# Optimization experiments

Measured on AMD Instinct MI355X. Metric: run time of the kernel, lower is better.

The kernel has to match this reference:

```python
import jax, jax.numpy as jnp
import numpy as np

N_EMBD = 2048
N_HEAD = 16
N_KV_HEAD = 4
HEAD_DIM = 128
KV_REPEATS = N_HEAD // N_KV_HEAD
ROPE_THETA = 10000.0


def rotate_half(x):
    # interleaved pair rotation: (x0,x1,x2,x3,...) -> (-x1,x0,-x3,x2,...)
    x_even = x[..., 0::2]
    x_odd = x[..., 1::2]
    return jnp.stack((-x_odd, x_even), axis=-1).reshape(x.shape)


def apply_rope(q, k, position_ids):
    inv_freq = 1.0 / (ROPE_THETA ** (jnp.arange(0, HEAD_DIM, 2, dtype=jnp.float32) / HEAD_DIM))
    freqs = position_ids.astype(jnp.float32)[:, None] * inv_freq[None, :]  # [S, D/2]
    emb = jnp.repeat(freqs, 2, axis=-1)  # [S, D] interleaved
    cos = jnp.cos(emb)[None, None, :, :]
    sin = jnp.sin(emb)[None, None, :, :]
    return q * cos + rotate_half(q) * sin, k * cos + rotate_half(k) * sin


def setup_inputs() -> dict:
    key = jax.random.key(0)
    ks = jax.random.split(key, 5)
    B, S = 2, 2048
    x = jax.random.normal(ks[0], (B, S, N_EMBD), dtype=jnp.float32)
    position_ids = jnp.arange(S, dtype=jnp.int32)
    scale = 0.02
    Wq = jax.random.normal(ks[1], (N_HEAD * HEAD_DIM, N_EMBD), dtype=jnp.float32) * scale
    Wk = jax.random.normal(ks[2], (N_KV_HEAD * HEAD_DIM, N_EMBD), dtype=jnp.float32) * scale
    Wv = jax.random.normal(ks[3], (N_KV_HEAD * HEAD_DIM, N_EMBD), dtype=jnp.float32) * scale
    Wo = jax.random.normal(ks[4], (N_EMBD, N_EMBD), dtype=jnp.float32) * scale
    return {"x": x, "Wq": Wq, "Wk": Wk, "Wv": Wv, "Wo": Wo, "position_ids": position_ids}


def reference(x, Wq, Wk, Wv, Wo, position_ids):
    B, S, _ = x.shape
    q = (x @ Wq.T).reshape(B, S, N_HEAD, HEAD_DIM).transpose(0, 2, 1, 3)      # [B,H,S,D]
    k = (x @ Wk.T).reshape(B, S, N_KV_HEAD, HEAD_DIM).transpose(0, 2, 1, 3)  # [B,Hkv,S,D]
    v = (x @ Wv.T).reshape(B, S, N_KV_HEAD, HEAD_DIM).transpose(0, 2, 1, 3)
    q, k = apply_rope(q, k, position_ids)
    # GQA: repeat kv heads consecutively
    k = jnp.repeat(k, KV_REPEATS, axis=1)  # [B,H,S,D]
    v = jnp.repeat(v, KV_REPEATS, axis=1)
    scores = jnp.einsum('bhqd,bhkd->bhqk', q, k) / jnp.sqrt(jnp.asarray(HEAD_DIM, q.dtype))
    key_positions = jnp.arange(S)
    mask = key_positions[None, :] > position_ids[:, None]  # [S, S]
    scores = jnp.where(mask[None, None, :, :], jnp.finfo(scores.dtype).min, scores)
    weights = jax.nn.softmax(scores.astype(jnp.float32), axis=-1).astype(q.dtype)
    y = jnp.einsum('bhqk,bhkd->bhqd', weights, v)
    y = y.transpose(0, 2, 1, 3).reshape(B, S, N_EMBD)
    return y @ Wo.T
```

## Files before the change

### kernel.cpp

```cpp
#include <hip/hip_runtime.h>
#include <stdint.h>

typedef unsigned short u16;
typedef unsigned int   u32;
typedef __attribute__((ext_vector_type(8))) short short8;
typedef __attribute__((ext_vector_type(4))) float f32x4;

#define S_LEN 2048
#define NEMB  2048
#define NH    16
#define NKV   4
#define HD    128
#define BATCH 2
#define MROWS (BATCH*S_LEN)

#define SCALE_Q 0.12751744f

__device__ __forceinline__ u16 f2bf(float f){
  u32 u = __float_as_uint(f);
  u += 0x7fffu + ((u>>16)&1u);
  return (u16)(u>>16);
}
__device__ __forceinline__ u16 f2bf_t(float f){
  return (u16)(__float_as_uint(f)>>16);
}
__device__ __forceinline__ float bf2f(u16 h){
  return __uint_as_float(((u32)h)<<16);
}
__device__ __forceinline__ float exp2_fast(float x){
  float r;
  asm("v_exp_f32 %0, %1" : "=v"(r) : "v"(x));
  return r;
}

typedef __attribute__((address_space(1))) const void gc_void;
typedef __attribute__((address_space(3))) void lds_void;
__device__ __forceinline__ void load_lds16(const void* g, void* l){
  __builtin_amdgcn_global_load_lds((gc_void*)(uintptr_t)g,
      (lds_void*)(u32)(uintptr_t)l, 16, 0, 0);
}

__global__ __launch_bounds__(256) void convert_kernel(
    const float* __restrict__ x, const float* __restrict__ wq,
    const float* __restrict__ wk, const float* __restrict__ wv,
    const float* __restrict__ wo,
    u16* __restrict__ xb, u16* __restrict__ wcb, u16* __restrict__ wob,
    const int* __restrict__ pos, float2* __restrict__ tab){
  const size_t NX=2097152, NWQ=1048576, NWK=262144, NWV=262144, NWO=1048576;
  const size_t total = NX+NWQ+NWK+NWV+NWO;
  for (size_t i = (size_t)blockIdx.x*blockDim.x + threadIdx.x; i < total;
       i += (size_t)gridDim.x*blockDim.x){
    const float* src; u16* dst; size_t j = i;
    if (j < NX){ src=x; dst=xb; }
    else { j-=NX;
      if (j<NWQ){ src=wq; dst=wcb; }
      else { j-=NWQ;
        if (j<NWK){ src=wk; dst=wcb+4194304; }
        else { j-=NWK;
          if (j<NWV){ src=wv; dst=wcb+5242880; }
          else { j-=NWV; src=wo; dst=wob; } } } }
    float4 v = *(const float4*)(src + j*4);
    u32 lo = (u32)f2bf(v.x) | ((u32)f2bf(v.y)<<16);
    u32 hi = (u32)f2bf(v.z) | ((u32)f2bf(v.w)<<16);
    uint2 pk; pk.x = lo; pk.y = hi;
    *(uint2*)(dst + j*4) = pk;
  }
  for (int id = blockIdx.x*blockDim.x + threadIdx.x; id < S_LEN*64;
       id += gridDim.x*blockDim.x){
    int s = id >> 6, i = id & 63;
    float p = (float)pos[s];
    float inv = __expf(-((float)(2*i)) * (1.0f/128.0f) * 9.210340371976184f);
    float f = p * inv;
    float sv, cv;
    sincosf(f, &sv, &cv);
    tab[id] = make_float2(cv, sv);
  }
}

__global__ __launch_bounds__(256) void transpose_v_kernel(const u16* __restrict__ vb,
                                                          u16* __restrict__ vt){
  __shared__ u16 tl[64][72];
  int bx = blockIdx.x;
  int m0 = (bx & 63)*64;
  int d0 = (bx >> 6)*64;
  int tid = threadIdx.x;
  #pragma unroll
  for (int i=0;i<2;i++){
    int t16 = i*256 + tid;
    int sl = t16 >> 3, dc = t16 & 7;
    *(uint4*)&tl[sl][dc*8] = *(const uint4*)&vb[(size_t)(m0+sl)*512 + d0 + dc*8];
  }
  __syncthreads();
  #pragma unroll
  for (int i=0;i<2;i++){
    int t16 = i*256 + tid;
    int sch = t16 >> 6, dl = t16 & 63;
    union { uint4 v; u16 e[8]; } O;
    #pragma unroll
    for (int j=0;j<8;j++) O.e[j] = tl[sch*8+j][dl];
    *(uint4*)&vt[(size_t)(d0+dl)*4096 + m0 + sch*8] = O.v;
  }
}

template<int EPI>
__global__ __launch_bounds__(256,3) void gemm128_kernel(
    const u16* __restrict__ A, const u16* __restrict__ B, int K,
    const float2* __restrict__ tab,
    u16* __restrict__ q_out, u16* __restrict__ k_out, u16* __restrict__ v_out,
    float* __restrict__ f_out){
  __shared__ u16 sA[2][128*32];
  __shared__ u16 sB[2][128*32];
  int tid = threadIdx.x;
  int wave = tid >> 6, lane = tid & 63;
  int lr = lane & 15, lc = lane >> 4;
  int wm = (wave>>1)*64, wn = (wave&1)*64;

  int nwgx = gridDim.x;
  int nwg  = nwgx * gridDim.y;
  int wg   = blockIdx.y*nwgx + blockIdx.x;
  wg = (wg & 7)*(nwg >> 3) + (wg >> 3);
  int bm = (wg / nwgx)*128, bn = (wg % nwgx)*128;

  const u16* Ag = A + (size_t)bm*K;
  const u16* Bg = B + (size_t)bn*K;

  auto stage = [&](int buf, int kt){
    const u16* Ak = Ag + kt*32;
    const u16* Bk = Bg + kt*32;
    #pragma unroll
    for (int rrd=0; rrd<2; ++rrd){
      int t16 = rrd*256 + tid;
      int row = t16 >> 2, ch = t16 & 3;
      u16* lb = &sA[buf][(size_t)(rrd*256 + (tid & 192))*8];
      load_lds16(Ak + (size_t)row*K + ch*8, lb);
    }
    #pragma unroll
    for (int rrd=0; rrd<2; ++rrd){
      int t16 = rrd*256 + tid;
      int row = t16 >> 2, ch = t16 & 3;
      u16* lb = &sB[buf][(size_t)(rrd*256 + (tid & 192))*8];
      load_lds16(Bk + (size_t)row*K + ch*8, lb);
    }
  };

  f32x4 acc[4][4];
  #pragma unroll
  for (int i=0;i<4;i++)
    #pragma unroll
    for (int j=0;j<4;j++) acc[i][j] = (f32x4)0.0f;

  stage(0,0);
  __syncthreads();
  int nk = K >> 5;
  int cur = 0;
  for (int kt=0; kt<nk; ++kt){
    if (kt+1 < nk) stage(cur^1, kt+1);
    short8 af[4], bfr[4];
    #pragma unroll
    for (int i=0;i<4;i++){
      af[i]  = *(const short8*)&sA[cur][(wm + i*16 + lr)*32 + lc*8];
      bfr[i] = *(const short8*)&sB[cur][(wn + i*16 + lr)*32 + lc*8];
    }
    __builtin_amdgcn_s_setprio(1);
    #pragma unroll
    for (int i=0;i<4;i++)
      #pragma unroll
      for (int j=0;j<4;j++)
        acc[i][j] = __builtin_amdgcn_mfma_f32_16x16x32_bf16(af[i], bfr[j], acc[i][j], 0,0,0);
    __builtin_amdgcn_s_setprio(0);
    __syncthreads();
    cur ^= 1;
  }

  #pragma unroll
  for (int i=0;i<4;i++){
    #pragma unroll
    for (int j=0;j<4;j++){
      #pragma unroll
      for (int r=0;r<4;r++){
        int m = bm + wm + i*16 + lc*4 + r;
        int n = bn + wn + j*16 + lr;
        float v = acc[i][j][r];
        if (EPI == 0){
          float p = __shfl_xor(v, 1);
          if (n < 2048){
            float2 cs = tab[((m & (S_LEN-1))<<6) + ((n & 127)>>1)];
            float o = (n & 1) ? (v*cs.x + p*cs.y) : (v*cs.x - p*cs.y);
            q_out[(size_t)m*2048 + n] = f2bf(o * SCALE_Q);
          } else if (n < 2560){
            int d = n - 2048;
            float2 cs = tab[((m & (S_LEN-1))<<6) + ((d & 127)>>1)];
            float o = (n & 1) ? (v*cs.x + p*cs.y) : (v*cs.x - p*cs.y);
            k_out[(size_t)m*512 + d] = f2bf(o);
          } else {
            v_out[(size_t)m*512 + (n-2560)] = f2bf(v);
          }
        } else {
          f_out[(size_t)m*2048 + n] = v;
        }
      }
    }
  }
}

__global__ __launch_bounds__(256,2) void attn_kernel(
    const u16* __restrict__ Q, const u16* __restrict__ Kb,
    const u16* __restrict__ Vt, u16* __restrict__ Y){
  __shared__ u16 sK[2][64*128];
  __shared__ u16 sVt[2][128*64];
  __shared__ u16 sP[4][16*64];

  int tid = threadIdx.x, wave = tid>>6, lane = tid&63;
  int lr = lane&15, lc = lane>>4;

  int bid = blockIdx.x;
  int kvg  = bid & 7;
  int rest = bid >> 3;
  int pj   = rest & 15;
  int hsub = rest >> 4;
  int b  = kvg >> 2;
  int hk = kvg & 3;
  int h  = hk*4 + hsub;

  const u16* Kg = Kb + (size_t)(b*S_LEN)*512 + hk*HD;
  const u16* Vg = Vt + (size_t)(hk*HD)*4096 + b*S_LEN;

  auto stage = [&](int buf, int kv0){
    #pragma unroll
    for (int i=0;i<4;i++){
      int t16 = i*256 + tid;
      int row = t16 >> 4, c = t16 & 15;
      int cgl = c ^ (row & 7);
      load_lds16(Kg + (size_t)(kv0+row)*512 + cgl*8,
                 &sK[buf][(size_t)(i*256 + (tid & 192))*8]);
    }
    #pragma unroll
    for (int i=0;i<4;i++){
      int t16 = i*256 + tid;
      int d = t16 >> 3, c = t16 & 7;
      int cgl = c ^ (d & 7);
      load_lds16(Vg + (size_t)d*4096 + kv0 + cgl*8,
                 &sVt[buf][(size_t)(i*256 + (tid & 192))*8]);
    }
  };

  char* spb = (char*)sP[wave];

  #pragma unroll 1
  for (int pass=0; pass<2; ++pass){
    int qt  = pass ? pj : (31 - pj);
    int q0  = qt*64;
    int qrb = q0 + wave*16;
    const u16* Qg = Q + (size_t)(b*S_LEN + qrb)*NEMB + h*HD;

    short8 qf[4];
    #pragma unroll
    for (int c=0;c<4;c++)
      qf[c] = *(const short8*)&Qg[(size_t)lr*NEMB + c*32 + lc*8];

    float m_run[4], l_run[4];
    #pragma unroll
    for (int r=0;r<4;r++){ m_run[r]=-1e30f; l_run[r]=0.0f; }
    f32x4 o[8];
    #pragma unroll
    for (int i=0;i<8;i++) o[i]=(f32x4)0.0f;

    int nt = qt + 1;
    stage(0,0);
    __syncthreads();
    int cur=0;
    for (int t=0;t<nt;++t){
      int kv0 = t*64;
      if (t+1<nt) stage(cur^1,(t+1)*64);

      f32x4 sc[4];
      #pragma unroll
      for (int c2=0;c2<4;c2++) sc[c2]=(f32x4)0.0f;
      const char* skb = (const char*)sK[cur];
      __builtin_amdgcn_s_setprio(1);
      #pragma unroll
      for (int c2=0;c2<4;c2++){
        int rr = c2*16 + lr;
        int xo = (rr&7)<<4;
        #pragma unroll
        for (int c=0;c<4;c++){
          int byteoff = (rr*256 + c*64 + lc*16) ^ xo;
          short8 kf = *(const short8*)(skb + byteoff);
          sc[c2] = __builtin_amdgcn_mfma_f32_16x16x32_bf16(qf[c], kf, sc[c2], 0,0,0);
        }
      }
      __builtin_amdgcn_s_setprio(0);

      if (t == nt-1){
        #pragma unroll
        for (int c2=0;c2<4;c2++){
          int kvgl = kv0 + c2*16 + lr;
          #pragma unroll
          for (int r=0;r<4;r++){
            int qg = qrb + lc*4 + r;
            if (kvgl > qg) sc[c2][r] = -1e30f;
          }
        }
      }

      float lmax[4];
      bool need = false;
      #pragma unroll
      for (int r=0;r<4;r++){
        lmax[r] = fmaxf(fmaxf(sc[0][r],sc[1][r]), fmaxf(sc[2][r],sc[3][r]));
        need = need || (lmax[r] > m_run[r] + 8.0f);
      }
      if (__any(need)){
        float fac[4];
        #pragma unroll
        for (int r=0;r<4;r++){
          float mm = lmax[r];
          mm = fmaxf(mm, __shfl_xor(mm,1));
          mm = fmaxf(mm, __shfl_xor(mm,2));
          mm = fmaxf(mm, __shfl_xor(mm,4));
          mm = fmaxf(mm, __shfl_xor(mm,8));
          float mn = fmaxf(m_run[r], mm);
          fac[r] = exp2_fast(m_run[r]-mn);
          m_run[r] = mn;
          l_run[r] *= fac[r];
        }
        #pragma unroll
        for (int i=0;i<8;i++)
          #pragma unroll
          for (int r=0;r<4;r++) o[i][r] *= fac[r];
      }
      #pragma unroll
      for (int r=0;r<4;r++){
        float p0 = exp2_fast(sc[0][r]-m_run[r]);
        float p1 = exp2_fast(sc[1][r]-m_run[r]);
        float p2 = exp2_fast(sc[2][r]-m_run[r]);
        float p3 = exp2_fast(sc[3][r]-m_run[r]);
        sc[0][r]=p0; sc[1][r]=p1; sc[2][r]=p2; sc[3][r]=p3;
        l_run[r] += (p0+p1)+(p2+p3);
      }

      #pragma unroll
      for (int c2=0;c2<4;c2++){
        #pragma unroll
        for (int r=0;r<4;r++){
          int row = lc*4+r;
          int byteoff = (row*128 + (c2*16+lr)*2) ^ ((row&7)<<4);
          *(u16*)(spb + byteoff) = f2bf_t(sc[c2][r]);
        }
      }
      short8 pa[2];
      {
        int xop = (lr&7)<<4;
        pa[0] = *(const short8*)(spb + ((lr*128 + lc*16) ^ xop));
        pa[1] = *(const short8*)(spb + ((lr*128 + 64 + lc*16) ^ xop));
      }

      const char* svb = (const char*)sVt[cur];
      __builtin_amdgcn_s_setprio(1);
      #pragma unroll
      for (int n=0;n<8;n++){
        int d = n*16+lr;
        int xo = (d&7)<<4;
        #pragma unroll
        for (int ks=0;ks<2;ks++){
          int byteoff = (d*128 + ks*64 + lc*16) ^ xo;
          short8 vf = *(const short8*)(svb + byteoff);
          o[n] = __builtin_amdgcn_mfma_f32_16x16x32_bf16(pa[ks], vf, o[n], 0,0,0);
        }
      }
      __builtin_amdgcn_s_setprio(0);

      __syncthreads();
      cur ^= 1;
    }

    float inv[4];
    #pragma unroll
    for (int r=0;r<4;r++){
      float s = l_run[r];
      s += __shfl_xor(s,1); s += __shfl_xor(s,2);
      s += __shfl_xor(s,4); s += __shfl_xor(s,8);
      inv[r] = __builtin_amdgcn_rcpf(s);
    }
    u16* Yg = Y + (size_t)(b*S_LEN + qrb)*NEMB + h*HD;
    #pragma unroll
    for (int n=0;n<8;n++){
      #pragma unroll
      for (int r=0;r<4;r++){
        float v = o[n][r] * inv[r];
        Yg[(size_t)(lc*4+r)*NEMB + n*16 + lr] = f2bf(v);
      }
    }
    __syncthreads();
  }
}

extern "C" void kernel_launch(void* const* d_in, const int* in_sizes, int n_in,
                              void* d_out, int out_size, void* d_ws, size_t ws_size,
                              hipStream_t stream){
  const float* x  = (const float*)d_in[0];
  const float* wq = (const float*)d_in[1];
  const float* wk = (const float*)d_in[2];
  const float* wv = (const float*)d_in[3];
  const float* wo = (const float*)d_in[4];
  const int*  pos = (const int*)d_in[5];
  float* out = (float*)d_out;

  char* ws = (char*)d_ws;
  size_t off = 0;
  auto alloc = [&](size_t bytes)->char*{
    char* p = ws + off; off += (bytes + 255) & ~(size_t)255; return p;
  };
  u16* xb  = (u16*)alloc(8388608ull*2);
  u16* wcb = (u16*)alloc(6291456ull*2);
  u16* wob = (u16*)alloc(4194304ull*2);
  u16* qb  = (u16*)alloc(8388608ull*2);
  u16* kb  = (u16*)alloc(2097152ull*2);
  u16* vb  = (u16*)alloc(2097152ull*2);
  u16* yb  = (u16*)alloc(8388608ull*2);
  float2* tab = (float2*)alloc((size_t)S_LEN*64*8);
  u16* vt = xb;

  convert_kernel<<<2048,256,0,stream>>>(x,wq,wk,wv,wo,xb,wcb,wob,pos,tab);
  gemm128_kernel<0><<<dim3(24,32),256,0,stream>>>(xb, wcb, 2048, tab, qb, kb, vb, nullptr);
  transpose_v_kernel<<<512,256,0,stream>>>(vb, vt);
  attn_kernel<<<512,256,0,stream>>>(qb, kb, vt, yb);
  gemm128_kernel<1><<<dim3(16,32),256,0,stream>>>(yb, wob, 2048, nullptr, nullptr,nullptr,nullptr, out);
}
```

Measured before the change: 292.8 us.

## Replace QKV projection GEMM with 256x256-tile 8-wave pipelined kernel

Adds a new QKV projection GEMM that computes 256x256 output tiles per 512-thread workgroup. It uses 128 KB of LDS with double-buffered direct-to-LDS loads, an XOR swizzle, and a ping-pong schedule that interleaves LDS reads, global stages and prioritized MFMA quadrants between barriers. The goal is more data reuse per tile and better overlap of memory with matrix math than the previous 128x128 kernel. The trade-offs are fewer workgroups (192), heavy register and LDS use, and many barriers. The RoPE, scaling and Q/K/V split epilogue is kept.

```diff
diff --git a/kernel.cpp b/kernel.cpp
--- a/kernel.cpp
+++ b/kernel.cpp
@@ -102,6 +102,195 @@
   }
 }
 
+#define BARR __builtin_amdgcn_s_barrier()
+#define WAITL0 asm volatile("s_waitcnt lgkmcnt(0)" ::: "memory")
+#define MFMA_QUAD(qm, qn) do { \
+  __builtin_amdgcn_s_setprio(1); \
+  _Pragma("unroll") \
+  for (int kk=0;kk<2;kk++) \
+    _Pragma("unroll") \
+    for (int mf=0;mf<4;mf++) \
+      _Pragma("unroll") \
+      for (int nf=0;nf<2;nf++) \
+        acc[(qm)*4+mf][(qn)*2+nf] = __builtin_amdgcn_mfma_f32_16x16x32_bf16( \
+            a[mf][kk], bb[qn][nf][kk], acc[(qm)*4+mf][(qn)*2+nf], 0,0,0); \
+  __builtin_amdgcn_s_setprio(0); } while(0)
+
+__global__ __launch_bounds__(512,2) void gemm256_kernel(
+    const u16* __restrict__ A, const u16* __restrict__ B, int K,
+    const float2* __restrict__ tab,
+    u16* __restrict__ q_out, u16* __restrict__ k_out, u16* __restrict__ v_out){
+  __shared__ char lds[131072];
+  int tid = threadIdx.x;
+  int lane = tid & 63, wid = tid >> 6;
+  int lr = lane & 15, lc = lane >> 4;
+  int wm2 = wid >> 2, wn4 = wid & 3;
+
+  const int NTX = 12;
+  int wg = (blockIdx.x & 7)*((NTX*16)>>3) + (blockIdx.x >> 3);
+  int bm = (wg / NTX)*256, bn = (wg % NTX)*256;
+
+  const u16* asrc[2]; const u16* bsrc[2];
+  u32 dstoff[2];
+  #pragma unroll
+  for (int i=0;i<2;i++){
+    int S = i*512 + tid;
+    int ridx = S>>3, c8 = S&7;
+    int c8s = c8 ^ (((ridx>>2)&1)<<1);
+    int arow = ((ridx>>6)<<7) | (ridx&63);
+    int bno  = ((ridx>>5)<<6) | (ridx&31);
+    asrc[i] = A + (size_t)(bm + arow)*K + c8s*8;
+    bsrc[i] = B + (size_t)(bn + bno)*K + c8s*8;
+    dstoff[i] = (u32)((i*512 + (tid & 448))*16);
+  }
+  auto stageA = [&](int p, int t, int h){
+    #pragma unroll
+    for (int i=0;i<2;i++)
+      load_lds16(asrc[i] + (size_t)(h*64)*K + t*64,
+                 lds + p*32768 + h*16384 + dstoff[i]);
+  };
+  auto stageB = [&](int p, int t, int h){
+    #pragma unroll
+    for (int i=0;i<2;i++)
+      load_lds16(bsrc[i] + (size_t)(h*32)*K + t*64,
+                 lds + 65536 + p*32768 + h*16384 + dstoff[i]);
+  };
+
+  u32 aoff[4][2], boff[2][2];
+  #pragma unroll
+  for (int mf=0; mf<4; mf++){
+    int ridx = wm2*64 + mf*16 + lr;
+    #pragma unroll
+    for (int kk=0; kk<2; kk++){
+      u32 byte = (u32)(ridx*128 + kk*64 + lc*16);
+      aoff[mf][kk] = byte ^ (u32)(((ridx>>2)&1)<<5);
+    }
+  }
+  #pragma unroll
+  for (int nf=0; nf<2; nf++){
+    int ridx = wn4*32 + nf*16 + lr;
+    #pragma unroll
+    for (int kk=0; kk<2; kk++){
+      u32 byte = (u32)(ridx*128 + kk*64 + lc*16);
+      boff[nf][kk] = byte ^ (u32)(((ridx>>2)&1)<<5);
+    }
+  }
+
+  f32x4 acc[8][4];
+  #pragma unroll
+  for (int i=0;i<8;i++)
+    #pragma unroll
+    for (int j=0;j<4;j++) acc[i][j] = (f32x4)0.0f;
+
+  short8 a[4][2], bb[2][2][2];
+  auto LDA = [&](int p, int h){
+    char* base = lds + p*32768 + h*16384;
+    #pragma unroll
+    for (int mf=0;mf<4;mf++)
+      #pragma unroll
+      for (int kk=0;kk<2;kk++)
+        a[mf][kk] = *(const short8*)(base + aoff[mf][kk]);
+  };
+  auto LDB = [&](int p, int h){
+    char* base = lds + 65536 + p*32768 + h*16384;
+    #pragma unroll
+    for (int nf=0;nf<2;nf++)
+      #pragma unroll
+      for (int kk=0;kk<2;kk++)
+        bb[h][nf][kk] = *(const short8*)(base + boff[nf][kk]);
+  };
+
+  int nk = K >> 6;
+
+  stageA(0,0,0); stageB(0,0,0); stageB(0,0,1); stageA(0,0,1);
+  asm volatile("s_waitcnt vmcnt(4)" ::: "memory");
+  stageA(1,1,0); stageB(1,1,0); stageB(1,1,1);
+  asm volatile("s_waitcnt vmcnt(6)" ::: "memory");
+  BARR;
+
+  for (int i = 0; i < (nk>>1); ++i){
+    int ta = 2*i, tb = 2*i+1;
+    bool s2 = (ta+2) < nk;
+
+    LDA(0,0); LDB(0,0);
+    stageA(1, tb, 1);
+    asm volatile("s_waitcnt lgkmcnt(8)" ::: "memory");
+    BARR; WAITL0;
+    MFMA_QUAD(0,0);
+    BARR;
+
+    LDB(0,1);
+    if (s2) stageA(0, ta+2, 0);
+    BARR; WAITL0;
+    MFMA_QUAD(0,1);
+    BARR;
+
+    LDA(0,1);
+    if (s2) stageB(0, ta+2, 0);
+    BARR; WAITL0;
+    MFMA_QUAD(1,0);
+    BARR;
+
+    if (s2) stageB(0, ta+2, 1);
+    BARR;
+    MFMA_QUAD(1,1);
+    if (s2) { asm volatile("s_waitcnt vmcnt(6)" ::: "memory"); }
+    else    { asm volatile("s_waitcnt vmcnt(0)" ::: "memory"); }
+    BARR;
+
+    LDA(1,0); LDB(1,0);
+    if (s2) stageA(0, ta+2, 1);
+    asm volatile("s_waitcnt lgkmcnt(8)" ::: "memory");
+    BARR; WAITL0;
+    MFMA_QUAD(0,0);
+    BARR;
+
+    LDB(1,1);
+    if (s2) stageA(1, tb+2, 0);
+    BARR; WAITL0;
+    MFMA_QUAD(0,1);
+    BARR;
+
+    LDA(1,1);
+    if (s2) stageB(1, tb+2, 0);
+    BARR; WAITL0;
+    MFMA_QUAD(1,0);
+    BARR;
+
+    if (s2) stageB(1, tb+2, 1);
+    BARR;
+    MFMA_QUAD(1,1);
+    asm volatile("s_waitcnt vmcnt(6)" ::: "memory");
+    BARR;
+  }
+
+  #pragma unroll
+  for (int mfi=0; mfi<8; mfi++){
+    #pragma unroll
+    for (int nfi=0; nfi<4; nfi++){
+      #pragma unroll
+      for (int r=0; r<4; r++){
+        int m = bm + wm2*128 + mfi*16 + lc*4 + r;
+        int n = bn + wn4*64 + nfi*16 + lr;
+        float v = acc[mfi][nfi][r];
+        float p = __shfl_xor(v, 1);
+        if (n < 2048){
+          float2 cs = tab[((m & (S_LEN-1))<<6) + ((n & 127)>>1)];
+          float o = (n & 1) ? (v*cs.x + p*cs.y) : (v*cs.x - p*cs.y);
+          q_out[(size_t)m*2048 + n] = f2bf(o * SCALE_Q);
+        } else if (n < 2560){
+          int d = n - 2048;
+          float2 cs = tab[((m & (S_LEN-1))<<6) + ((d & 127)>>1)];
+          float o = (n & 1) ? (v*cs.x + p*cs.y) : (v*cs.x - p*cs.y);
+          k_out[(size_t)m*512 + d] = f2bf(o);
+        } else {
+          v_out[(size_t)m*512 + (n-2560)] = f2bf(v);
+        }
+      }
+    }
+  }
+}
+
 template<int EPI>
 __global__ __launch_bounds__(256,3) void gemm128_kernel(
     const u16* __restrict__ A, const u16* __restrict__ B, int K,
@@ -422,7 +611,7 @@
   u16* vt = xb;
 
   convert_kernel<<<2048,256,0,stream>>>(x,wq,wk,wv,wo,xb,wcb,wob,pos,tab);
-  gemm128_kernel<0><<<dim3(24,32),256,0,stream>>>(xb, wcb, 2048, tab, qb, kb, vb, nullptr);
+  gemm256_kernel<<<192,512,0,stream>>>(xb, wcb, 2048, tab, qb, kb, vb);
   transpose_v_kernel<<<512,256,0,stream>>>(vb, vt);
   attn_kernel<<<512,256,0,stream>>>(qb, kb, vt, yb);
   gemm128_kernel<1><<<dim3(16,32),256,0,stream>>>(yb, wob, 2048, nullptr, nullptr,nullptr,nullptr, out);
```

New measurement: 321.7 us. +9.9%, slower.
